# Kernel optimization log

Hardware: AMD Instinct MI355X
Metric: run time of the kernel (lower is better)

Reference implementation:

```python
import jax, jax.numpy as jnp
import numpy as np

N = 50000      # nodes
E = 600000     # edges
D = 128        # dim_h == num_features
G = 512        # graphs in batch
BN_EPS = 1e-5


def _w(k, shape, fan_in):
    return jax.random.normal(k, shape, jnp.float32) * np.float32(1.0 / np.sqrt(fan_in))


def setup_inputs() -> dict:
    key = jax.random.key(0)
    ks = jax.random.split(key, 16)
    return {
        "x": jax.random.normal(ks[0], (N, D), jnp.float32),
        "edge_index": jax.random.randint(ks[1], (2, E), 0, N, jnp.int64),
        "batch": jnp.sort(jax.random.randint(ks[2], (N,), 0, G, jnp.int64)),
        # GINConv 1 MLP: Linear -> BN -> ReLU -> Linear -> ReLU
        "c1_W1": _w(ks[3], (D, D), D), "c1_b1": jnp.zeros((D,), jnp.float32),
        "c1_g": jnp.ones((D,), jnp.float32), "c1_be": jnp.zeros((D,), jnp.float32),
        "c1_W2": _w(ks[4], (D, D), D), "c1_b2": jnp.zeros((D,), jnp.float32),
        # GINConv 2 MLP
        "c2_W1": _w(ks[5], (D, D), D), "c2_b1": jnp.zeros((D,), jnp.float32),
        "c2_g": jnp.ones((D,), jnp.float32), "c2_be": jnp.zeros((D,), jnp.float32),
        "c2_W2": _w(ks[6], (D, D), D), "c2_b2": jnp.zeros((D,), jnp.float32),
        # readout MLP
        "lin1_W": _w(ks[7], (4 * D, 4 * D), 4 * D), "lin1_b": jnp.zeros((4 * D,), jnp.float32),
        "lin2_W": _w(ks[8], (4 * D, 1), 4 * D), "lin2_b": jnp.zeros((1,), jnp.float32),
    }


def _gin_conv(x, src, dst, W1, b1, g, be, W2, b2):
    # sum aggregation of neighbor messages (PyG GINConv, eps=0)
    agg = jax.ops.segment_sum(x[src], dst, num_segments=x.shape[0])
    h = (agg + x) @ W1 + b1
    # BatchNorm1d, training mode (biased batch stats over nodes)
    mu = h.mean(axis=0)
    var = h.var(axis=0)
    h = jax.nn.relu(g * (h - mu) * jax.lax.rsqrt(var + BN_EPS) + be)
    return jax.nn.relu(h @ W2 + b2)


def _pool(h, batch):
    add = jax.ops.segment_sum(h, batch, num_segments=G)
    mx = jax.ops.segment_max(h, batch, num_segments=G)
    mx = jnp.where(jnp.isfinite(mx), mx, 0.0)  # empty segments -> 0
    return add, mx


def reference(x, edge_index, batch,
              c1_W1, c1_b1, c1_g, c1_be, c1_W2, c1_b2,
              c2_W1, c2_b1, c2_g, c2_be, c2_W2, c2_b2,
              lin1_W, lin1_b, lin2_W, lin2_b):
    src, dst = edge_index[0], edge_index[1]
    h1 = _gin_conv(x, src, dst, c1_W1, c1_b1, c1_g, c1_be, c1_W2, c1_b2)
    h2 = _gin_conv(h1, src, dst, c2_W1, c2_b1, c2_g, c2_be, c2_W2, c2_b2)
    a1, m1 = _pool(h1, batch)
    a2, m2 = _pool(h2, batch)
    h = jnp.concatenate([a1, a2, m1, m2], axis=1)  # [G, 4D]
    h = jax.nn.relu(h @ lin1_W + lin1_b)
    h = h @ lin2_W + lin2_b  # [G, 1]
    return jax.nn.sigmoid(h), h
```

## Files before the change

kernel.cpp:

```cpp
#include <hip/hip_runtime.h>

#define D 128
#define GNUM 512

typedef _Float16 f16;
typedef _Float16 f16x8 __attribute__((ext_vector_type(8)));
typedef float f32x4 __attribute__((ext_vector_type(4)));

__global__ void deg_kernel(const int* __restrict__ ei, int* __restrict__ deg,
                           int nE) {
  int e = blockIdx.x * blockDim.x + threadIdx.x;
  if (e < nE) atomicAdd(&deg[ei[nE + e]], 1);
}

__global__ __launch_bounds__(256) void partial_kernel(
    const int* __restrict__ deg, int* __restrict__ partials, int n) {
  __shared__ int sh[256];
  const int t = threadIdx.x;
  const int i = blockIdx.x * 512 + t * 2;
  int s = 0;
  if (i < n) s += deg[i];
  if (i + 1 < n) s += deg[i + 1];
  sh[t] = s;
  __syncthreads();
#pragma unroll
  for (int off = 128; off > 0; off >>= 1) {
    if (t < off) sh[t] += sh[t + off];
    __syncthreads();
  }
  if (t == 0) partials[blockIdx.x] = sh[0];
}

__global__ __launch_bounds__(128) void scanp_kernel(
    int* __restrict__ partials, int nP, int* __restrict__ rowptr, int n,
    int nE) {
  __shared__ int sh[128];
  const int t = threadIdx.x;
  const int v = (t < nP) ? partials[t] : 0;
  sh[t] = v;
  __syncthreads();
#pragma unroll
  for (int off = 1; off < 128; off <<= 1) {
    int u = (t >= off) ? sh[t - off] : 0;
    __syncthreads();
    sh[t] += u;
    __syncthreads();
  }
  if (t < nP) partials[t] = sh[t] - v;
  if (t == 0) rowptr[n] = nE;
}

__global__ __launch_bounds__(256) void emit_kernel(
    const int* __restrict__ deg, const int* __restrict__ partials,
    int* __restrict__ rowptr, int* __restrict__ cursor, int n) {
  __shared__ int sh[256];
  const int t = threadIdx.x;
  const int i = blockIdx.x * 512 + t * 2;
  const int d0 = (i < n) ? deg[i] : 0;
  const int d1 = (i + 1 < n) ? deg[i + 1] : 0;
  const int s = d0 + d1;
  sh[t] = s;
  __syncthreads();
#pragma unroll
  for (int off = 1; off < 256; off <<= 1) {
    int u = (t >= off) ? sh[t - off] : 0;
    __syncthreads();
    sh[t] += u;
    __syncthreads();
  }
  int base = partials[blockIdx.x] + sh[t] - s;
  if (i < n) {
    rowptr[i] = base;
    cursor[i] = base;
    base += d0;
  }
  if (i + 1 < n) {
    rowptr[i + 1] = base;
    cursor[i + 1] = base;
  }
}

__global__ void fill_kernel(const int* __restrict__ ei, int* __restrict__ cursor,
                            int* __restrict__ csr, int nE) {
  int e = blockIdx.x * blockDim.x + threadIdx.x;
  if (e < nE) {
    int d = ei[nE + e];
    int pos = atomicAdd(&cursor[d], 1);
    csr[pos] = ei[e];
  }
}

__global__ void gstart_kernel(const int* __restrict__ batch,
                              int* __restrict__ gstart, int n) {
  int g = blockIdx.x * blockDim.x + threadIdx.x;
  if (g > GNUM) return;
  if (g == GNUM) { gstart[g] = n; return; }
  int lo = 0, hi = n;
  while (lo < hi) {
    int mid = (lo + hi) >> 1;
    if (batch[mid] < g) lo = mid + 1; else hi = mid;
  }
  gstart[g] = lo;
}

__global__ void xcvt_kernel(const float* __restrict__ in, f16* __restrict__ out,
                            int n4) {
  int i = blockIdx.x * 256 + threadIdx.x;
  if (i < n4) {
    float4 v = ((const float4*)in)[i];
    union { f16 h[4]; uint2 u; } p;
    p.h[0] = (f16)v.x; p.h[1] = (f16)v.y; p.h[2] = (f16)v.z; p.h[3] = (f16)v.w;
    ((uint2*)out)[i] = p.u;
  }
}

__global__ void wprep_kernel(const float* __restrict__ W0,
                             const float* __restrict__ W1,
                             const float* __restrict__ W2,
                             const float* __restrict__ W3,
                             f16* __restrict__ out) {
  int idx = blockIdx.x * 256 + threadIdx.x;
  int wsel = idx >> 14;
  int rem = idx & 16383;
  int col = rem >> 7, k = rem & 127;
  const float* W = (wsel == 0) ? W0 : (wsel == 1) ? W1 : (wsel == 2) ? W2 : W3;
  out[idx] = (f16)W[k * D + col];
}

__global__ __launch_bounds__(256) void agg16_kernel(
    const f16* __restrict__ feat, const int* __restrict__ rowptr,
    const int* __restrict__ csr, f16* __restrict__ out, int n) {
  int row = blockIdx.x * 16 + (threadIdx.x >> 4);
  int q = threadIdx.x & 15;
  if (row >= n) return;
  const int co = q * 8;
  float a[8];
  f16x8 v = *(const f16x8*)(feat + (size_t)row * D + co);
#pragma unroll
  for (int j = 0; j < 8; j++) a[j] = (float)v[j];
  int beg = rowptr[row], end = rowptr[row + 1];
  int i = beg;
  for (; i + 1 < end; i += 2) {
    int s0 = csr[i], s1 = csr[i + 1];
    f16x8 v0 = *(const f16x8*)(feat + (size_t)s0 * D + co);
    f16x8 v1 = *(const f16x8*)(feat + (size_t)s1 * D + co);
#pragma unroll
    for (int j = 0; j < 8; j++) a[j] += (float)v0[j] + (float)v1[j];
  }
  if (i < end) {
    f16x8 v0 = *(const f16x8*)(feat + (size_t)csr[i] * D + co);
#pragma unroll
    for (int j = 0; j < 8; j++) a[j] += (float)v0[j];
  }
  f16x8 o;
#pragma unroll
  for (int j = 0; j < 8; j++) o[j] = (f16)a[j];
  *(f16x8*)(out + (size_t)row * D + co) = o;
}

template <int BN, int OUT>
__global__ __launch_bounds__(64) void gemm16_kernel(
    const f16* __restrict__ A, const float* __restrict__ ss,
    const f16* __restrict__ WT, const float* __restrict__ bias,
    f16* __restrict__ C, float* __restrict__ pstat, int n) {
  const int l = threadIdx.x;
  const int rw0 = blockIdx.x * 32;
  const int lr = l & 15;
  const int lq = l >> 4;
  const int lk = lq * 8;

  f32x4 acc[2][8];
#pragma unroll
  for (int m = 0; m < 2; m++)
#pragma unroll
    for (int nt = 0; nt < 8; nt++) acc[m][nt] = (f32x4)0.f;

#pragma unroll
  for (int s = 0; s < 4; s++) {
    const int k = s * 32 + lk;
    f16x8 af[2];
#pragma unroll
    for (int m = 0; m < 2; m++) {
      int row = rw0 + m * 16 + lr;
      f16x8 v = (f16x8)(f16)0.f;
      if (row < n) v = *(const f16x8*)(A + (size_t)row * D + k);
      if (BN) {
        float4 c0 = *(const float4*)(ss + k);
        float4 c1 = *(const float4*)(ss + k + 4);
        float4 h0 = *(const float4*)(ss + 128 + k);
        float4 h1 = *(const float4*)(ss + 128 + k + 4);
        f16x8 r;
        r[0] = (f16)fmaxf(0.f, fmaf((float)v[0], c0.x, h0.x));
        r[1] = (f16)fmaxf(0.f, fmaf((float)v[1], c0.y, h0.y));
        r[2] = (f16)fmaxf(0.f, fmaf((float)v[2], c0.z, h0.z));
        r[3] = (f16)fmaxf(0.f, fmaf((float)v[3], c0.w, h0.w));
        r[4] = (f16)fmaxf(0.f, fmaf((float)v[4], c1.x, h1.x));
        r[5] = (f16)fmaxf(0.f, fmaf((float)v[5], c1.y, h1.y));
        r[6] = (f16)fmaxf(0.f, fmaf((float)v[6], c1.z, h1.z));
        r[7] = (f16)fmaxf(0.f, fmaf((float)v[7], c1.w, h1.w));
        af[m] = r;
      } else {
        af[m] = v;
      }
    }
    f16x8 bf[8];
#pragma unroll
    for (int nt = 0; nt < 8; nt++) {
      int col = nt * 16 + lr;
      bf[nt] = *(const f16x8*)(WT + (size_t)col * D + k);
    }
#pragma unroll
    for (int m = 0; m < 2; m++)
#pragma unroll
      for (int nt = 0; nt < 8; nt++)
        acc[m][nt] = __builtin_amdgcn_mfma_f32_16x16x32_f16(af[m], bf[nt],
                                                            acc[m][nt], 0, 0, 0);
  }

  if constexpr (OUT == 0) {
    float ts[8], tq[8];
#pragma unroll
    for (int nt = 0; nt < 8; nt++) { ts[nt] = 0.f; tq[nt] = 0.f; }
#pragma unroll
    for (int m = 0; m < 2; m++)
#pragma unroll
      for (int r = 0; r < 4; r++) {
        int row = rw0 + m * 16 + lq * 4 + r;
        if (row < n) {
#pragma unroll
          for (int nt = 0; nt < 8; nt++) {
            float v = acc[m][nt][r] + bias[nt * 16 + lr];
            C[(size_t)row * D + nt * 16 + lr] = (f16)v;
            ts[nt] += v;
            tq[nt] = fmaf(v, v, tq[nt]);
          }
        }
      }
#pragma unroll
    for (int nt = 0; nt < 8; nt++) {
      ts[nt] += __shfl_xor(ts[nt], 16); ts[nt] += __shfl_xor(ts[nt], 32);
      tq[nt] += __shfl_xor(tq[nt], 16); tq[nt] += __shfl_xor(tq[nt], 32);
    }
    if (l < 16) {
      float* ps = pstat + (size_t)blockIdx.x * 256;
#pragma unroll
      for (int nt = 0; nt < 8; nt++) {
        ps[nt * 16 + l] = ts[nt];
        ps[128 + nt * 16 + l] = tq[nt];
      }
    }
  } else {
#pragma unroll
    for (int m = 0; m < 2; m++)
#pragma unroll
      for (int r = 0; r < 4; r++) {
        int row = rw0 + m * 16 + lq * 4 + r;
        if (row < n) {
#pragma unroll
          for (int nt = 0; nt < 8; nt++) {
            float v = fmaxf(0.f, acc[m][nt][r] + bias[nt * 16 + lr]);
            C[(size_t)row * D + nt * 16 + lr] = (f16)v;
          }
        }
      }
  }
}

__global__ __launch_bounds__(256) void statreduce_kernel(
    const float* __restrict__ pstat, float* __restrict__ colsum, int nB) {
  int c = threadIdx.x;
  float s = 0.f;
  for (int b = blockIdx.x; b < nB; b += gridDim.x)
    s += pstat[(size_t)b * 256 + c];
  atomicAdd(colsum + c, s);
}

__global__ void bnstats_kernel(const float* __restrict__ colsum,
                               const float* __restrict__ g,
                               const float* __restrict__ be,
                               float* __restrict__ ss, int n) {
  int c = threadIdx.x;
  float inv_n = 1.0f / (float)n;
  float mean = colsum[c] * inv_n;
  float var = colsum[128 + c] * inv_n - mean * mean;
  float scale = g[c] * rsqrtf(var + 1e-5f);
  ss[c] = scale;
  ss[128 + c] = be[c] - mean * scale;
}

__global__ __launch_bounds__(256) void pool2_kernel(
    const f16* __restrict__ h1, const f16* __restrict__ h2,
    const int* __restrict__ gstart, float* __restrict__ pooled) {
  int g = blockIdx.x;
  int c = threadIdx.x & 127;
  int half = threadIdx.x >> 7;
  int r0 = gstart[g], r1 = gstart[g + 1];
  float s1 = 0.f, m1 = 0.f, s2 = 0.f, m2 = 0.f;
  for (int r = r0 + half; r < r1; r += 2) {
    float v1 = (float)h1[(size_t)r * D + c];
    float v2 = (float)h2[(size_t)r * D + c];
    s1 += v1; m1 = fmaxf(m1, v1);
    s2 += v2; m2 = fmaxf(m2, v2);
  }
  __shared__ float sh[256];
  sh[threadIdx.x] = s1; __syncthreads();
  if (half == 0) s1 += sh[threadIdx.x + 128];
  __syncthreads(); sh[threadIdx.x] = s2; __syncthreads();
  if (half == 0) s2 += sh[threadIdx.x + 128];
  __syncthreads(); sh[threadIdx.x] = m1; __syncthreads();
  if (half == 0) m1 = fmaxf(m1, sh[threadIdx.x + 128]);
  __syncthreads(); sh[threadIdx.x] = m2; __syncthreads();
  if (half == 0) {
    m2 = fmaxf(m2, sh[threadIdx.x + 128]);
    float* pg = pooled + (size_t)g * 512;
    pg[c] = s1;
    pg[128 + c] = s2;
    pg[256 + c] = m1;
    pg[384 + c] = m2;
  }
}

__global__ __launch_bounds__(512) void lin1_kernel(
    const float* __restrict__ pooled, const float* __restrict__ W,
    float* __restrict__ out1) {
  __shared__ float prow[4][128];
  const int j = threadIdx.x;
  const int gt = blockIdx.x >> 2;
  const int kt = blockIdx.x & 3;
  const int g0 = gt * 4, k0 = kt * 128;
  prow[j >> 7][j & 127] = pooled[(size_t)(g0 + (j >> 7)) * 512 + k0 + (j & 127)];
  __syncthreads();
  float acc[4] = {0.f, 0.f, 0.f, 0.f};
  for (int k = 0; k < 128; k++) {
    float w = W[(size_t)(k0 + k) * 512 + j];
#pragma unroll
    for (int r = 0; r < 4; r++) acc[r] = fmaf(prow[r][k], w, acc[r]);
  }
#pragma unroll
  for (int r = 0; r < 4; r++)
    atomicAdd(out1 + (size_t)(g0 + r) * 512 + j, acc[r]);
}

__global__ void lin2_kernel(const float* __restrict__ out1,
                            const float* __restrict__ b1,
                            const float* __restrict__ W,
                            const float* __restrict__ b2,
                            float* __restrict__ out) {
  int g = blockIdx.x;
  int lane = threadIdx.x;
  float s = 0.f;
  for (int k = lane; k < 512; k += 64)
    s = fmaf(fmaxf(0.f, out1[(size_t)g * 512 + k] + b1[k]), W[k], s);
#pragma unroll
  for (int off = 32; off > 0; off >>= 1) s += __shfl_down(s, off);
  if (lane == 0) {
    float h = s + b2[0];
    out[g] = 1.0f / (1.0f + expf(-h));
    out[GNUM + g] = h;
  }
}

extern "C" void kernel_launch(void* const* d_in, const int* in_sizes, int n_in,
                              void* d_out, int out_size, void* d_ws,
                              size_t ws_size, hipStream_t stream) {
  const float* x = (const float*)d_in[0];
  const int* ei = (const int*)d_in[1];
  const int* batch = (const int*)d_in[2];
  const float* c1_W1 = (const float*)d_in[3];
  const float* c1_b1 = (const float*)d_in[4];
  const float* c1_g  = (const float*)d_in[5];
  const float* c1_be = (const float*)d_in[6];
  const float* c1_W2 = (const float*)d_in[7];
  const float* c1_b2 = (const float*)d_in[8];
  const float* c2_W1 = (const float*)d_in[9];
  const float* c2_b1 = (const float*)d_in[10];
  const float* c2_g  = (const float*)d_in[11];
  const float* c2_be = (const float*)d_in[12];
  const float* c2_W2 = (const float*)d_in[13];
  const float* c2_b2 = (const float*)d_in[14];
  const float* lin1_W = (const float*)d_in[15];
  const float* lin1_b = (const float*)d_in[16];
  const float* lin2_W = (const float*)d_in[17];
  const float* lin2_b = (const float*)d_in[18];

  const int n = in_sizes[0] / D;
  const int nE = in_sizes[1] / 2;

  char* p = (char*)d_ws;
  auto take = [&](size_t bytes) {
    char* r = p;
    p += (bytes + 255) & ~(size_t)255;
    return r;
  };
  f16*   hpre   = (f16*)take((size_t)n * D * 2);
  f16*   aggt   = (f16*)take((size_t)n * D * 2);
  f16*   h1     = (f16*)take((size_t)n * D * 2);
  f16*   wt     = (f16*)take(4 * 16384 * 2);
  float* pooled = (float*)take((size_t)GNUM * 512 * 4);
  float* out1b  = (float*)take((size_t)GNUM * 512 * 4);
  float* colsum = (float*)take(256 * 4);
  int*   gstart = (int*)take((GNUM + 1) * 4);
  int* deg      = (int*)take((size_t)n * 4);
  int* rowptr   = (int*)take((size_t)(n + 1) * 4);
  int* cursor   = (int*)take((size_t)(n + 1) * 4);
  int* partials = (int*)take(128 * 4);
  int* csr      = (int*)take((size_t)nE * 4);
  const int nB = (n + 31) / 32;
  float* pstat  = (float*)take((size_t)nB * 256 * 4);

  const int edge_grid = (nE + 255) / 256;
  const int agg_grid = (n + 15) / 16;
  const int nP = (n + 511) / 512;
  const int n4 = n * D / 4;

  hipMemsetAsync(deg, 0, (size_t)n * sizeof(int), stream);
  hipMemsetAsync(out1b, 0, (size_t)GNUM * 512 * sizeof(float), stream);
  deg_kernel<<<edge_grid, 256, 0, stream>>>(ei, deg, nE);
  partial_kernel<<<nP, 256, 0, stream>>>(deg, partials, n);
  scanp_kernel<<<1, 128, 0, stream>>>(partials, nP, rowptr, n, nE);
  emit_kernel<<<nP, 256, 0, stream>>>(deg, partials, rowptr, cursor, n);
  fill_kernel<<<edge_grid, 256, 0, stream>>>(ei, cursor, csr, nE);
  gstart_kernel<<<3, 256, 0, stream>>>(batch, gstart, n);
  wprep_kernel<<<256, 256, 0, stream>>>(c1_W1, c1_W2, c2_W1, c2_W2, wt);
  xcvt_kernel<<<(n4 + 255) / 256, 256, 0, stream>>>(x, h1, n4);

  agg16_kernel<<<agg_grid, 256, 0, stream>>>(h1, rowptr, csr, aggt, n);
  gemm16_kernel<0, 0><<<nB, 64, 0, stream>>>(aggt, nullptr, wt, c1_b1, hpre,
                                             pstat, n);
  hipMemsetAsync(colsum, 0, 256 * sizeof(float), stream);
  statreduce_kernel<<<32, 256, 0, stream>>>(pstat, colsum, nB);
  bnstats_kernel<<<1, 128, 0, stream>>>(colsum, c1_g, c1_be, colsum, n);
  gemm16_kernel<1, 1><<<nB, 64, 0, stream>>>(hpre, colsum, wt + 16384, c1_b2,
                                             h1, nullptr, n);

  agg16_kernel<<<agg_grid, 256, 0, stream>>>(h1, rowptr, csr, aggt, n);
  gemm16_kernel<0, 0><<<nB, 64, 0, stream>>>(aggt, nullptr, wt + 32768, c2_b1,
                                             hpre, pstat, n);
  hipMemsetAsync(colsum, 0, 256 * sizeof(float), stream);
  statreduce_kernel<<<32, 256, 0, stream>>>(pstat, colsum, nB);
  bnstats_kernel<<<1, 128, 0, stream>>>(colsum, c2_g, c2_be, colsum, n);
  gemm16_kernel<1, 1><<<nB, 64, 0, stream>>>(hpre, colsum, wt + 49152, c2_b2,
                                             aggt, nullptr, n);

  pool2_kernel<<<GNUM, 256, 0, stream>>>(h1, aggt, gstart, pooled);
  lin1_kernel<<<512, 512, 0, stream>>>(pooled, lin1_W, out1b);
  lin2_kernel<<<GNUM, 64, 0, stream>>>(out1b, lin1_b, lin2_W, lin2_b,
                                       (float*)d_out);
}
```

Baseline: 279.2 us.

## Split agg accumulators, shrink GEMM tiles, drop memsets and atomic stat reduction

The aggregation kernel now walks two halves of each neighbor list with independent accumulators to expose more memory-level parallelism. The GEMM kernel processes 16 rows per block instead of 32, doubling the grid to raise occupancy at the cost of reloading weights more often. The BN statistic reduction replaces atomics plus per-layer memsets with a two-stage deterministic reduction. The deg and out1b memsets are merged into one by placing the buffers next to each other.

```diff
diff --git a/kernel.cpp b/kernel.cpp
--- a/kernel.cpp
+++ b/kernel.cpp
@@ -134,27 +134,29 @@
   int q = threadIdx.x & 15;
   if (row >= n) return;
   const int co = q * 8;
-  float a[8];
+  float a[8], b[8];
   f16x8 v = *(const f16x8*)(feat + (size_t)row * D + co);
 #pragma unroll
-  for (int j = 0; j < 8; j++) a[j] = (float)v[j];
-  int beg = rowptr[row], end = rowptr[row + 1];
-  int i = beg;
-  for (; i + 1 < end; i += 2) {
-    int s0 = csr[i], s1 = csr[i + 1];
-    f16x8 v0 = *(const f16x8*)(feat + (size_t)s0 * D + co);
+  for (int j = 0; j < 8; j++) { a[j] = (float)v[j]; b[j] = 0.f; }
+  const int beg = rowptr[row], end = rowptr[row + 1];
+  const int len = end - beg;
+  const int half = len >> 1;
+  int j1 = beg, j2 = beg + half;
+  for (int it = 0; it < half; it++, j1++, j2++) {
+    int s1 = csr[j1], s2 = csr[j2];
     f16x8 v1 = *(const f16x8*)(feat + (size_t)s1 * D + co);
-#pragma unroll
-    for (int j = 0; j < 8; j++) a[j] += (float)v0[j] + (float)v1[j];
-  }
-  if (i < end) {
-    f16x8 v0 = *(const f16x8*)(feat + (size_t)csr[i] * D + co);
-#pragma unroll
-    for (int j = 0; j < 8; j++) a[j] += (float)v0[j];
+    f16x8 v2 = *(const f16x8*)(feat + (size_t)s2 * D + co);
+#pragma unroll
+    for (int j = 0; j < 8; j++) { a[j] += (float)v1[j]; b[j] += (float)v2[j]; }
+  }
+  if (len & 1) {
+    f16x8 v1 = *(const f16x8*)(feat + (size_t)csr[end - 1] * D + co);
+#pragma unroll
+    for (int j = 0; j < 8; j++) a[j] += (float)v1[j];
   }
   f16x8 o;
 #pragma unroll
-  for (int j = 0; j < 8; j++) o[j] = (f16)a[j];
+  for (int j = 0; j < 8; j++) o[j] = (f16)(a[j] + b[j]);
   *(f16x8*)(out + (size_t)row * D + co) = o;
 }
 
@@ -164,78 +166,64 @@
     const f16* __restrict__ WT, const float* __restrict__ bias,
     f16* __restrict__ C, float* __restrict__ pstat, int n) {
   const int l = threadIdx.x;
-  const int rw0 = blockIdx.x * 32;
+  const int rw0 = blockIdx.x * 16;
   const int lr = l & 15;
   const int lq = l >> 4;
   const int lk = lq * 8;
 
-  f32x4 acc[2][8];
-#pragma unroll
-  for (int m = 0; m < 2; m++)
-#pragma unroll
-    for (int nt = 0; nt < 8; nt++) acc[m][nt] = (f32x4)0.f;
+  f32x4 acc[8];
+#pragma unroll
+  for (int nt = 0; nt < 8; nt++) acc[nt] = (f32x4)0.f;
 
 #pragma unroll
   for (int s = 0; s < 4; s++) {
     const int k = s * 32 + lk;
-    f16x8 af[2];
-#pragma unroll
-    for (int m = 0; m < 2; m++) {
-      int row = rw0 + m * 16 + lr;
-      f16x8 v = (f16x8)(f16)0.f;
-      if (row < n) v = *(const f16x8*)(A + (size_t)row * D + k);
-      if (BN) {
-        float4 c0 = *(const float4*)(ss + k);
-        float4 c1 = *(const float4*)(ss + k + 4);
-        float4 h0 = *(const float4*)(ss + 128 + k);
-        float4 h1 = *(const float4*)(ss + 128 + k + 4);
-        f16x8 r;
-        r[0] = (f16)fmaxf(0.f, fmaf((float)v[0], c0.x, h0.x));
-        r[1] = (f16)fmaxf(0.f, fmaf((float)v[1], c0.y, h0.y));
-        r[2] = (f16)fmaxf(0.f, fmaf((float)v[2], c0.z, h0.z));
-        r[3] = (f16)fmaxf(0.f, fmaf((float)v[3], c0.w, h0.w));
-        r[4] = (f16)fmaxf(0.f, fmaf((float)v[4], c1.x, h1.x));
-        r[5] = (f16)fmaxf(0.f, fmaf((float)v[5], c1.y, h1.y));
-        r[6] = (f16)fmaxf(0.f, fmaf((float)v[6], c1.z, h1.z));
-        r[7] = (f16)fmaxf(0.f, fmaf((float)v[7], c1.w, h1.w));
-        af[m] = r;
-      } else {
-        af[m] = v;
+    const int row = rw0 + lr;
+    f16x8 af = (f16x8)(f16)0.f;
+    if (row < n) af = *(const f16x8*)(A + (size_t)row * D + k);
+    if (BN) {
+      float4 c0 = *(const float4*)(ss + k);
+      float4 c1 = *(const float4*)(ss + k + 4);
+      float4 h0 = *(const float4*)(ss + 128 + k);
+      float4 h1 = *(const float4*)(ss + 128 + k + 4);
+      f16x8 r;
+      r[0] = (f16)fmaxf(0.f, fmaf((float)af[0], c0.x, h0.x));
+      r[1] = (f16)fmaxf(0.f, fmaf((float)af[1], c0.y, h0.y));
+      r[2] = (f16)fmaxf(0.f, fmaf((float)af[2], c0.z, h0.z));
+      r[3] = (f16)fmaxf(0.f, fmaf((float)af[3], c0.w, h0.w));
+      r[4] = (f16)fmaxf(0.f, fmaf((float)af[4], c1.x, h1.x));
+      r[5] = (f16)fmaxf(0.f, fmaf((float)af[5], c1.y, h1.y));
+      r[6] = (f16)fmaxf(0.f, fmaf((float)af[6], c1.z, h1.z));
+      r[7] = (f16)fmaxf(0.f, fmaf((float)af[7], c1.w, h1.w));
+      af = r;
+    }
+    f16x8 bf[8];
+#pragma unroll
+    for (int nt = 0; nt < 8; nt++)
+      bf[nt] = *(const f16x8*)(WT + (size_t)(nt * 16 + lr) * D + k);
+#pragma unroll
+    for (int nt = 0; nt < 8; nt++)
+      acc[nt] = __builtin_amdgcn_mfma_f32_16x16x32_f16(af, bf[nt], acc[nt],
+                                                       0, 0, 0);
+  }
+
+  if constexpr (OUT == 0) {
+    float ts[8], tq[8];
+#pragma unroll
+    for (int nt = 0; nt < 8; nt++) { ts[nt] = 0.f; tq[nt] = 0.f; }
+#pragma unroll
+    for (int r = 0; r < 4; r++) {
+      int row = rw0 + lq * 4 + r;
+      if (row < n) {
+#pragma unroll
+        for (int nt = 0; nt < 8; nt++) {
+          float v = acc[nt][r] + bias[nt * 16 + lr];
+          C[(size_t)row * D + nt * 16 + lr] = (f16)v;
+          ts[nt] += v;
+          tq[nt] = fmaf(v, v, tq[nt]);
+        }
       }
     }
-    f16x8 bf[8];
-#pragma unroll
-    for (int nt = 0; nt < 8; nt++) {
-      int col = nt * 16 + lr;
-      bf[nt] = *(const f16x8*)(WT + (size_t)col * D + k);
-    }
-#pragma unroll
-    for (int m = 0; m < 2; m++)
-#pragma unroll
-      for (int nt = 0; nt < 8; nt++)
-        acc[m][nt] = __builtin_amdgcn_mfma_f32_16x16x32_f16(af[m], bf[nt],
-                                                            acc[m][nt], 0, 0, 0);
-  }
-
-  if constexpr (OUT == 0) {
-    float ts[8], tq[8];
-#pragma unroll
-    for (int nt = 0; nt < 8; nt++) { ts[nt] = 0.f; tq[nt] = 0.f; }
-#pragma unroll
-    for (int m = 0; m < 2; m++)
-#pragma unroll
-      for (int r = 0; r < 4; r++) {
-        int row = rw0 + m * 16 + lq * 4 + r;
-        if (row < n) {
-#pragma unroll
-          for (int nt = 0; nt < 8; nt++) {
-            float v = acc[m][nt][r] + bias[nt * 16 + lr];
-            C[(size_t)row * D + nt * 16 + lr] = (f16)v;
-            ts[nt] += v;
-            tq[nt] = fmaf(v, v, tq[nt]);
-          }
-        }
-      }
 #pragma unroll
     for (int nt = 0; nt < 8; nt++) {
       ts[nt] += __shfl_xor(ts[nt], 16); ts[nt] += __shfl_xor(ts[nt], 32);
@@ -251,38 +239,42 @@
     }
   } else {
 #pragma unroll
-    for (int m = 0; m < 2; m++)
-#pragma unroll
-      for (int r = 0; r < 4; r++) {
-        int row = rw0 + m * 16 + lq * 4 + r;
-        if (row < n) {
-#pragma unroll
-          for (int nt = 0; nt < 8; nt++) {
-            float v = fmaxf(0.f, acc[m][nt][r] + bias[nt * 16 + lr]);
-            C[(size_t)row * D + nt * 16 + lr] = (f16)v;
-          }
+    for (int r = 0; r < 4; r++) {
+      int row = rw0 + lq * 4 + r;
+      if (row < n) {
+#pragma unroll
+        for (int nt = 0; nt < 8; nt++) {
+          float v = fmaxf(0.f, acc[nt][r] + bias[nt * 16 + lr]);
+          C[(size_t)row * D + nt * 16 + lr] = (f16)v;
         }
       }
+    }
   }
 }
 
 __global__ __launch_bounds__(256) void statreduce_kernel(
-    const float* __restrict__ pstat, float* __restrict__ colsum, int nB) {
+    const float* __restrict__ pstat, float* __restrict__ pstat2, int nB) {
   int c = threadIdx.x;
   float s = 0.f;
-  for (int b = blockIdx.x; b < nB; b += gridDim.x)
+  for (int b = blockIdx.x; b < nB; b += 32)
     s += pstat[(size_t)b * 256 + c];
-  atomicAdd(colsum + c, s);
-}
-
-__global__ void bnstats_kernel(const float* __restrict__ colsum,
+  pstat2[(size_t)blockIdx.x * 256 + c] = s;
+}
+
+__global__ void bnstats_kernel(const float* __restrict__ pstat2,
                                const float* __restrict__ g,
                                const float* __restrict__ be,
                                float* __restrict__ ss, int n) {
   int c = threadIdx.x;
+  float s = 0.f, sq = 0.f;
+#pragma unroll
+  for (int i = 0; i < 32; i++) {
+    s += pstat2[i * 256 + c];
+    sq += pstat2[i * 256 + 128 + c];
+  }
   float inv_n = 1.0f / (float)n;
-  float mean = colsum[c] * inv_n;
-  float var = colsum[128 + c] * inv_n - mean * mean;
+  float mean = s * inv_n;
+  float var = sq * inv_n - mean * mean;
   float scale = g[c] * rsqrtf(var + 1e-5f);
   ss[c] = scale;
   ss[128 + c] = be[c] - mean * scale;
@@ -398,23 +390,23 @@
   f16*   wt     = (f16*)take(4 * 16384 * 2);
   float* pooled = (float*)take((size_t)GNUM * 512 * 4);
   float* out1b  = (float*)take((size_t)GNUM * 512 * 4);
-  float* colsum = (float*)take(256 * 4);
+  int*   deg    = (int*)take((size_t)n * 4);
+  float* ssbuf  = (float*)take(256 * 4);
   int*   gstart = (int*)take((GNUM + 1) * 4);
-  int* deg      = (int*)take((size_t)n * 4);
   int* rowptr   = (int*)take((size_t)(n + 1) * 4);
   int* cursor   = (int*)take((size_t)(n + 1) * 4);
   int* partials = (int*)take(128 * 4);
   int* csr      = (int*)take((size_t)nE * 4);
-  const int nB = (n + 31) / 32;
+  const int nB = (n + 15) / 16;
   float* pstat  = (float*)take((size_t)nB * 256 * 4);
+  float* pstat2 = (float*)take(32 * 256 * 4);
 
   const int edge_grid = (nE + 255) / 256;
   const int agg_grid = (n + 15) / 16;
   const int nP = (n + 511) / 512;
   const int n4 = n * D / 4;
 
-  hipMemsetAsync(deg, 0, (size_t)n * sizeof(int), stream);
-  hipMemsetAsync(out1b, 0, (size_t)GNUM * 512 * sizeof(float), stream);
+  hipMemsetAsync(out1b, 0, (size_t)GNUM * 512 * 4 + (size_t)n * 4, stream);
   deg_kernel<<<edge_grid, 256, 0, stream>>>(ei, deg, nE);
   partial_kernel<<<nP, 256, 0, stream>>>(deg, partials, n);
   scanp_kernel<<<1, 128, 0, stream>>>(partials, nP, rowptr, n, nE);
@@ -427,19 +419,17 @@
   agg16_kernel<<<agg_grid, 256, 0, stream>>>(h1, rowptr, csr, aggt, n);
   gemm16_kernel<0, 0><<<nB, 64, 0, stream>>>(aggt, nullptr, wt, c1_b1, hpre,
                                              pstat, n);
-  hipMemsetAsync(colsum, 0, 256 * sizeof(float), stream);
-  statreduce_kernel<<<32, 256, 0, stream>>>(pstat, colsum, nB);
-  bnstats_kernel<<<1, 128, 0, stream>>>(colsum, c1_g, c1_be, colsum, n);
-  gemm16_kernel<1, 1><<<nB, 64, 0, stream>>>(hpre, colsum, wt + 16384, c1_b2,
+  statreduce_kernel<<<32, 256, 0, stream>>>(pstat, pstat2, nB);
+  bnstats_kernel<<<1, 128, 0, stream>>>(pstat2, c1_g, c1_be, ssbuf, n);
+  gemm16_kernel<1, 1><<<nB, 64, 0, stream>>>(hpre, ssbuf, wt + 16384, c1_b2,
                                              h1, nullptr, n);
 
   agg16_kernel<<<agg_grid, 256, 0, stream>>>(h1, rowptr, csr, aggt, n);
   gemm16_kernel<0, 0><<<nB, 64, 0, stream>>>(aggt, nullptr, wt + 32768, c2_b1,
                                              hpre, pstat, n);
-  hipMemsetAsync(colsum, 0, 256 * sizeof(float), stream);
-  statreduce_kernel<<<32, 256, 0, stream>>>(pstat, colsum, nB);
-  bnstats_kernel<<<1, 128, 0, stream>>>(colsum, c2_g, c2_be, colsum, n);
-  gemm16_kernel<1, 1><<<nB, 64, 0, stream>>>(hpre, colsum, wt + 49152, c2_b2,
+  statreduce_kernel<<<32, 256, 0, stream>>>(pstat, pstat2, nB);
+  bnstats_kernel<<<1, 128, 0, stream>>>(pstat2, c2_g, c2_be, ssbuf, n);
+  gemm16_kernel<1, 1><<<nB, 64, 0, stream>>>(hpre, ssbuf, wt + 49152, c2_b2,
                                              aggt, nullptr, n);
 
   pool2_kernel<<<GNUM, 256, 0, stream>>>(h1, aggt, gstart, pooled);
```

New measurement: 313.4 us. 1.12x slower.
